# Performance work log

Measured on AMD Instinct MI355X. Metric: run time of the kernel, lower is better.

Reference implementation:

```python
import jax, jax.numpy as jnp
import numpy as np

NUM_HEADS = 8

def setup_inputs() -> dict:
    key = jax.random.key(0)
    ks = jax.random.split(key, 12)
    B, C, H, W = 4, 256, 64, 64
    QK = 256
    NSP = 256
    x = jax.random.normal(ks[0], (B, C, H, W), dtype=jnp.float32)
    affinity_matrix = jax.random.uniform(ks[1], (B, NSP, H * W), dtype=jnp.float32)
    norm_w = 1.0 + 0.02 * jax.random.normal(ks[2], (C,), dtype=jnp.float32)
    norm_b = 0.02 * jax.random.normal(ks[3], (C,), dtype=jnp.float32)
    Wq = 0.02 * jax.random.normal(ks[4], (QK, C), dtype=jnp.float32)
    Wk = 0.02 * jax.random.normal(ks[5], (QK, C), dtype=jnp.float32)
    Wv = 0.02 * jax.random.normal(ks[6], (C, C), dtype=jnp.float32)
    Wsp = 0.02 * jax.random.normal(ks[7], (QK, C), dtype=jnp.float32)
    lepe_w = 0.02 * jax.random.normal(ks[8], (C, 1, 3, 3), dtype=jnp.float32)  # depthwise OIHW
    lepe_b = 0.02 * jax.random.normal(ks[9], (C,), dtype=jnp.float32)
    return {"x": x, "affinity_matrix": affinity_matrix, "norm_w": norm_w,
            "norm_b": norm_b, "Wq": Wq, "Wk": Wk, "Wv": Wv, "Wsp": Wsp,
            "lepe_w": lepe_w, "lepe_b": lepe_b, "num_spixels": NSP}


def _layernorm2d(x, w, b, eps=1e-6):
    # LayerNorm over channel dim of NCHW input
    xp = x.transpose(0, 2, 3, 1)  # B,H,W,C
    mu = xp.mean(-1, keepdims=True)
    var = ((xp - mu) ** 2).mean(-1, keepdims=True)
    xn = (xp - mu) * jax.lax.rsqrt(var + eps) * w + b
    return xn.transpose(0, 3, 1, 2)


def _sgca(x, affinity_matrix, norm_w, norm_b, Wq, Wk, Wv, Wsp, lepe_w, lepe_b, num_spixels):
    B, C, H, W = x.shape
    HW = H * W
    h = NUM_HEADS
    qk_dim = Wq.shape[0]
    dqk = qk_dim // h
    dv = C // h
    scale = (C // h) ** -0.5

    xn = _layernorm2d(x, norm_w, norm_b)

    # superpixel aggregation: b (hw) c
    x_flat = xn.reshape(B, C, HW).transpose(0, 2, 1)  # B,HW,C
    stoken = jnp.einsum('bmn,bnc->bmc', affinity_matrix, x_flat)
    stoken = stoken / (affinity_matrix.sum(-1, keepdims=True) + 1e-16)  # B,nsp,C

    # sp projection -> B,h,dqk,nsp
    st = jnp.einsum('bmc,qc->bmq', stoken, Wsp).transpose(0, 2, 1)
    st = st.reshape(B, h, dqk, num_spixels)

    # 1x1 conv projections
    q = jnp.einsum('oc,bchw->bohw', Wq, xn).reshape(B, h, dqk, HW)
    k = jnp.einsum('oc,bchw->bohw', Wk, xn).reshape(B, h, dqk, HW)
    vx = jnp.einsum('oc,bchw->bohw', Wv, xn)  # B,C,H,W
    v = vx.reshape(B, h, dv, HW)

    # LePE: depthwise 3x3 conv on v(x)
    lepe = jax.lax.conv_general_dilated(
        vx, lepe_w, window_strides=(1, 1), padding=((1, 1), (1, 1)),
        feature_group_count=C, dimension_numbers=('NCHW', 'OIHW', 'NCHW'))
    lepe = lepe + lepe_b[None, :, None, None]
    # faithful to original: [B,C,HW] -> permute -> [B,HW,C] -> reshape B,C,H,W
    lepe = lepe.reshape(B, C, HW).transpose(0, 2, 1).reshape(B, C, H, W)

    # stage 1: k^T @ stoken, softmax over HW axis
    s_attn = jnp.einsum('bhdn,bhdm->bhnm', k, st) * scale  # B,h,HW,nsp
    s_attn = jax.nn.softmax(s_attn, axis=-2)
    s_out = jnp.einsum('bhdn,bhnm->bhdm', v, s_attn)  # B,h,dv,nsp

    # stage 2: stoken^T @ q, softmax over nsp axis
    x_attn = jnp.einsum('bhdm,bhdn->bhmn', st, q) * scale  # B,h,nsp,HW
    x_attn = jax.nn.softmax(x_attn, axis=-2)
    x_out = jnp.einsum('bhdm,bhmn->bhdn', s_out, x_attn).reshape(B, C, H, W)

    return x_out + lepe


def reference(x, affinity_matrix, norm_w, norm_b, Wq, Wk, Wv, Wsp, lepe_w, lepe_b, num_spixels):
    return _sgca(x, affinity_matrix, norm_w, norm_b, Wq, Wk, Wv, Wsp, lepe_w, lepe_b, num_spixels)
```

## Files before the change

kernel.cpp:

```cpp
#include <hip/hip_runtime.h>
#include <hip/hip_bf16.h>

#define BATCH 4
#define CCH   256
#define HWHW  4096
#define NSP   256
#define NHEAD 8
#define SCALE 0.17677669529663689f
#define PLANE 1048576L

typedef short bf16x8 __attribute__((ext_vector_type(8)));
typedef float f32x4  __attribute__((ext_vector_type(4)));

__global__ __launch_bounds__(256)
void ln_fused_kernel(const float* __restrict__ x, const float* __restrict__ w,
                     const float* __restrict__ bb,
                     const float* __restrict__ Wq, const float* __restrict__ Wk,
                     const float* __restrict__ Wv, const float* __restrict__ Wsp,
                     const float* __restrict__ aff,
                     __hip_bfloat16* __restrict__ xn_cn,
                     __hip_bfloat16* __restrict__ xn_nc,
                     __hip_bfloat16* __restrict__ wbf,
                     __hip_bfloat16* __restrict__ aff_bf)
{
    __shared__ __hip_bfloat16 xs[256][72];
    __shared__ float ps[4][64], pss[4][64], mus[64], rstds[64];
    __shared__ float wls[256], bls[256];
    int blk = blockIdx.x;
    int t = threadIdx.x;
    if (blk >= 256) {
        int sel = blk - 256;
        if (sel < 4) {
            const float* src = (sel == 0) ? Wq : (sel == 1) ? Wk : (sel == 2) ? Wv : Wsp;
            __hip_bfloat16* dst = wbf + sel * 65536;
            for (int i = t * 4; i < 65536; i += 1024) {
                float4 f = *(const float4*)(src + i);
                __hip_bfloat16 p[4];
                p[0] = __float2bfloat16(f.x); p[1] = __float2bfloat16(f.y);
                p[2] = __float2bfloat16(f.z); p[3] = __float2bfloat16(f.w);
                *(int2*)(dst + i) = *(int2*)p;
            }
        } else {
            long base = (long)(sel - 4) * 65536;
            for (int i = t * 4; i < 65536; i += 1024) {
                float4 f = *(const float4*)(aff + base + i);
                __hip_bfloat16 p[4];
                p[0] = __float2bfloat16(f.x); p[1] = __float2bfloat16(f.y);
                p[2] = __float2bfloat16(f.z); p[3] = __float2bfloat16(f.w);
                *(int2*)(aff_bf + base + i) = *(int2*)p;
            }
        }
        return;
    }
    int b = blk >> 6;
    int n0 = (blk & 63) * 64;
    int p = t & 63, cq = t >> 6;
    wls[t] = w[t]; bls[t] = bb[t];
    long base = (long)b * CCH * HWHW + n0 + p;
    float s = 0.f, ss = 0.f;
#pragma unroll 8
    for (int i = 0; i < 64; ++i) {
        int c = cq * 64 + i;
        float v = x[base + (long)c * HWHW];
        xs[c][p] = __float2bfloat16(v);
        s += v; ss += v * v;
    }
    ps[cq][p] = s; pss[cq][p] = ss;
    __syncthreads();
    if (cq == 0) {
        float S  = ps[0][p] + ps[1][p] + ps[2][p] + ps[3][p];
        float SS = pss[0][p] + pss[1][p] + pss[2][p] + pss[3][p];
        float mu = S * (1.f / 256.f);
        float var = SS * (1.f / 256.f) - mu * mu;
        mus[p] = mu; rstds[p] = rsqrtf(var + 1e-6f);
    }
    __syncthreads();
    float mu = mus[p], rstd = rstds[p];
#pragma unroll
    for (int c8 = 0; c8 < 8; ++c8) {
        short pack[8];
#pragma unroll
        for (int j = 0; j < 8; ++j) {
            int c = cq * 64 + c8 * 8 + j;
            float v = ((float)xs[c][p] - mu) * rstd * wls[c] + bls[c];
            __hip_bfloat16 bv = __float2bfloat16(v);
            xs[c][p] = bv;
            pack[j] = *(short*)&bv;
        }
        *(int4*)(xn_nc + ((long)b * HWHW + n0 + p) * CCH + cq * 64 + c8 * 8) = *(int4*)pack;
    }
    __syncthreads();
#pragma unroll
    for (int i = 0; i < 8; ++i) {
        int idx = t + i * 256;
        int c = idx >> 3, seg = idx & 7;
        *(int4*)(xn_cn + (long)(b * CCH + c) * HWHW + n0 + seg * 8) =
            *(const int4*)&xs[c][seg * 8];
    }
}

__global__ __launch_bounds__(256)
void reduce8_cast_kernel(const float* __restrict__ part, const float* __restrict__ rsPart,
                         __hip_bfloat16* __restrict__ out, float* __restrict__ rs)
{
    int i = blockIdx.x * 256 + threadIdx.x;
    if (blockIdx.x < 4) {
        int b = i >> 8, m = i & 255;
        float s = 0.f;
#pragma unroll
        for (int ch = 0; ch < 8; ++ch) s += rsPart[((b * 8 + ch) << 8) + m];
        rs[i] = s;
    }
    int b = i >> 16, idx = i & 65535;
    long base = (long)b * 8 * 65536 + idx;
    float s = 0.f;
#pragma unroll
    for (int ch = 0; ch < 8; ++ch) s += part[base + (long)ch * 65536];
    out[i] = __float2bfloat16(s);
}

template <int OUTK, bool ROWSCALE, bool ROWSUM>
__global__ __launch_bounds__(256)
void mfma_gemm_nt(const __hip_bfloat16* __restrict__ A, const __hip_bfloat16* __restrict__ B,
                  void* __restrict__ Cptr, int N, int K, int kChunk, int kShift,
                  long aStrideZ, long bStrideZ, long cStrideZ,
                  const float* __restrict__ rowScale, long sStrideZ,
                  float* __restrict__ rsPart)
{
    __shared__ __hip_bfloat16 Asm[4 * 64 * 8];
    __shared__ __hip_bfloat16 Bsm[4 * 64 * 8];
    int z = blockIdx.z;
    int b = z >> kShift;
    int ch = z & ((1 << kShift) - 1);
    int t = threadIdx.x;
    int lane = t & 63, w = t >> 6;
    int l15 = lane & 15, quad = lane >> 4;
    int Mt = blockIdx.y * 64, Nt = blockIdx.x * 64;

    const __hip_bfloat16* aSrc = A + b * aStrideZ + (long)ch * kChunk
        + (long)(Mt + w * 16 + l15) * K + quad * 8;
    const __hip_bfloat16* bSrc = B + b * bStrideZ + (long)ch * kChunk
        + (long)(Nt + w * 16 + l15) * K + quad * 8;
    __hip_bfloat16* aDst = &Asm[t * 8];
    __hip_bfloat16* bDst = &Bsm[t * 8];

    f32x4 acc00 = {0.f,0.f,0.f,0.f}, acc01 = acc00, acc10 = acc00, acc11 = acc00;
    f32x4 rs0 = acc00, rs1 = acc00;
    bf16x8 onesf;
    { short o = (l15 == 0) ? (short)0x3F80 : (short)0;
      onesf = bf16x8{o, o, o, o, o, o, o, o}; }
    int wm = (w & 1) * 2, wn = (w >> 1) * 2;

    int4 aReg = *(const int4*)aSrc;
    int4 bReg = *(const int4*)bSrc;
    for (int k0 = 0; k0 < kChunk; k0 += 32) {
        *(int4*)aDst = aReg;
        *(int4*)bDst = bReg;
        __syncthreads();
        if (k0 + 32 < kChunk) {
            aSrc += 32; bSrc += 32;
            aReg = *(const int4*)aSrc;
            bReg = *(const int4*)bSrc;
        }
        bf16x8 a0 = ((const bf16x8*)Asm)[wm * 64 + lane];
        bf16x8 a1 = ((const bf16x8*)Asm)[(wm + 1) * 64 + lane];
        bf16x8 b0 = ((const bf16x8*)Bsm)[wn * 64 + lane];
        bf16x8 b1 = ((const bf16x8*)Bsm)[(wn + 1) * 64 + lane];
        acc00 = __builtin_amdgcn_mfma_f32_16x16x32_bf16(a0, b0, acc00, 0, 0, 0);
        acc01 = __builtin_amdgcn_mfma_f32_16x16x32_bf16(a0, b1, acc01, 0, 0, 0);
        acc10 = __builtin_amdgcn_mfma_f32_16x16x32_bf16(a1, b0, acc10, 0, 0, 0);
        acc11 = __builtin_amdgcn_mfma_f32_16x16x32_bf16(a1, b1, acc11, 0, 0, 0);
        if (ROWSUM) {
            rs0 = __builtin_amdgcn_mfma_f32_16x16x32_bf16(a0, onesf, rs0, 0, 0, 0);
            rs1 = __builtin_amdgcn_mfma_f32_16x16x32_bf16(a1, onesf, rs1, 0, 0, 0);
        }
        __syncthreads();
    }
    if (ROWSUM && blockIdx.x == 0 && (w >> 1) == 0 && l15 == 0) {
#pragma unroll
        for (int r = 0; r < 4; ++r) {
            rsPart[(long)z * 256 + Mt + wm * 16 + quad * 4 + r]       = rs0[r];
            rsPart[(long)z * 256 + Mt + (wm + 1) * 16 + quad * 4 + r] = rs1[r];
        }
    }
    f32x4 accs[2][2] = {{acc00, acc01}, {acc10, acc11}};
#pragma unroll
    for (int i = 0; i < 2; ++i)
#pragma unroll
        for (int j = 0; j < 2; ++j)
#pragma unroll
            for (int r = 0; r < 4; ++r) {
                int m = Mt + (wm + i) * 16 + quad * 4 + r;
                int n = Nt + (wn + j) * 16 + l15;
                float val = accs[i][j][r];
                if (ROWSCALE) val /= (rowScale[(long)b * sStrideZ + m] + 1e-16f);
                long off = (long)z * cStrideZ + (long)m * N + n;
                if (OUTK == 0) ((float*)Cptr)[off] = val;
                else ((__hip_bfloat16*)Cptr)[off] = __float2bfloat16(val);
            }
}

__global__ __launch_bounds__(256)
void stage1_mfma(const __hip_bfloat16* __restrict__ qk_nc,
                 const __hip_bfloat16* __restrict__ v_cn,
                 const __hip_bfloat16* __restrict__ st_md,
                 __hip_bfloat16* __restrict__ opart)
{
    __shared__ __hip_bfloat16 Es[256 * 72];
    __shared__ __hip_bfloat16 sts[256 * 40];
    const int chunk = blockIdx.x, bh = blockIdx.y;
    const int b = bh >> 3, h = bh & 7;
    const int t = threadIdx.x, lane = t & 63, w = t >> 6;
    const int l15 = lane & 15, quad = lane >> 4;
    const int n0 = chunk * 256;

    {
        const int4* src = (const int4*)(st_md + ((long)(b * 256 + t)) * 256 + h * 32);
        int4* dst = (int4*)&sts[t * 40];
        dst[0] = src[0]; dst[1] = src[1]; dst[2] = src[2]; dst[3] = src[3];
    }
    __syncthreads();
    bf16x8 afrag[16];
#pragma unroll
    for (int mt = 0; mt < 16; ++mt)
        afrag[mt] = *(const bf16x8*)&sts[(mt * 16 + l15) * 40 + quad * 8];
    bf16x8 onesf;
    { short o = (l15 == 0) ? (short)0x3F80 : (short)0;
      onesf = bf16x8{o, o, o, o, o, o, o, o}; }

    f32x4 occ[4][3];
#pragma unroll
    for (int i = 0; i < 4; ++i)
#pragma unroll
        for (int j = 0; j < 3; ++j) occ[i][j] = f32x4{0.f,0.f,0.f,0.f};

    for (int sub = 0; sub < 4; ++sub) {
        const int nbase = n0 + sub * 64;
        bf16x8 kf = *(const bf16x8*)(qk_nc + ((long)b * 4096 + nbase + 16 * w + l15) * 512 + 256 + h * 32 + quad * 8);
#pragma unroll
        for (int mt = 0; mt < 16; ++mt) {
            f32x4 s = __builtin_amdgcn_mfma_f32_16x16x32_bf16(afrag[mt], kf, f32x4{0.f,0.f,0.f,0.f}, 0, 0, 0);
#pragma unroll
            for (int r = 0; r < 4; ++r)
                Es[(mt * 16 + quad * 4 + r) * 72 + 16 * w + l15] =
                    __float2bfloat16(__expf(s[r] * SCALE));
        }
        __syncthreads();
#pragma unroll
        for (int ks = 0; ks < 2; ++ks) {
            bf16x8 bf0 = *(const bf16x8*)(v_cn + ((long)(b * 256 + h * 32 + l15)) * 4096 + nbase + ks * 32 + quad * 8);
            bf16x8 bf1 = *(const bf16x8*)(v_cn + ((long)(b * 256 + h * 32 + 16 + l15)) * 4096 + nbase + ks * 32 + quad * 8);
#pragma unroll
            for (int mi = 0; mi < 4; ++mi) {
                bf16x8 af = *(const bf16x8*)&Es[(64 * w + mi * 16 + l15) * 72 + ks * 32 + quad * 8];
                occ[mi][0] = __builtin_amdgcn_mfma_f32_16x16x32_bf16(af, bf0, occ[mi][0], 0, 0, 0);
                occ[mi][1] = __builtin_amdgcn_mfma_f32_16x16x32_bf16(af, bf1, occ[mi][1], 0, 0, 0);
                occ[mi][2] = __builtin_amdgcn_mfma_f32_16x16x32_bf16(af, onesf, occ[mi][2], 0, 0, 0);
            }
        }
        __syncthreads();
    }
    __hip_bfloat16* tb = Es;
#pragma unroll
    for (int mi = 0; mi < 4; ++mi)
#pragma unroll
        for (int jt = 0; jt < 3; ++jt) {
            if (jt == 2 && l15 != 0) continue;
            int col = jt * 16 + l15;
#pragma unroll
            for (int r = 0; r < 4; ++r) {
                int m = 64 * w + mi * 16 + quad * 4 + r;
                tb[col * 264 + m] = __float2bfloat16(occ[mi][jt][r]);
            }
        }
    __syncthreads();
    int* og = (int*)(opart) + (long)(chunk * 32 + bh) * 4224;
    const int* tbi = (const int*)tb;
#pragma unroll
    for (int i = 0; i < 17; ++i) {
        int idx = t + i * 256;
        if (idx < 4224) {
            int row = idx >> 7, off = idx & 127;
            og[idx] = tbi[row * 132 + off];
        }
    }
}

__global__ __launch_bounds__(256)
void merge1_kernel(const __hip_bfloat16* __restrict__ opart, __hip_bfloat16* __restrict__ sout)
{
    int t = blockIdx.x * 256 + threadIdx.x;
    int m = t & 255;
    int d = (t >> 8) & 31;
    int bh = t >> 13;
    float num = 0.f, den = 0.f;
    for (int ch = 0; ch < 16; ++ch) {
        long base = (long)((ch * 32 + bh) * 33) * 256 + m;
        num += (float)opart[base + (long)d * 256];
        den += (float)opart[base + 32 * 256];
    }
    sout[(long)bh * 8192 + d * 256 + m] = __float2bfloat16(num / den);
}

__global__ __launch_bounds__(256)
void lepe_conv_t_kernel(const __hip_bfloat16* __restrict__ v_cn,
                        const float* __restrict__ lw, const float* __restrict__ lb,
                        __hip_bfloat16* __restrict__ lepe_cn)
{
    __shared__ __hip_bfloat16 in_t[32 * 384];
    __shared__ __hip_bfloat16 tile_bf[256 * 33];
    __shared__ float wls[288], bls[32];
    const int bx = blockIdx.x;
    const int c0 = blockIdx.y * 32;
    const int b  = blockIdx.z;
    const int t = threadIdx.x;
    const int n0 = bx * 256, r0 = bx * 4;

    for (int i = t; i < 288; i += 256) wls[i] = lw[c0 * 9 + i];
    if (t < 32)  bls[t] = lb[c0 + t];
#pragma unroll
    for (int i = 0; i < 6; ++i) {
        int vi = t + i * 256;
        int ch = vi / 48;
        int off = (vi % 48) * 8;
        int g = (r0 - 1) * 64 + off;
        int4 val = {0, 0, 0, 0};
        if ((unsigned)g < 4096u)
            val = *(const int4*)(v_cn + (((long)(b * CCH + c0 + ch)) << 12) + g);
        *(int4*)&in_t[ch * 384 + off] = val;
    }
    __syncthreads();

    const int lane = t & 63, w = t >> 6;
#pragma unroll
    for (int i = 0; i < 8; ++i) {
        int ch = w * 8 + i;
        float cr[6], lf[6], rf[6];
#pragma unroll
        for (int rr = 0; rr < 6; ++rr) {
            cr[rr] = (float)in_t[ch * 384 + rr * 64 + lane];
            float lv = __shfl_up(cr[rr], 1);
            float rv = __shfl_down(cr[rr], 1);
            lf[rr] = (lane == 0) ? 0.f : lv;
            rf[rr] = (lane == 63) ? 0.f : rv;
        }
        float w0 = wls[ch*9+0], w1 = wls[ch*9+1], w2 = wls[ch*9+2];
        float w3 = wls[ch*9+3], w4 = wls[ch*9+4], w5 = wls[ch*9+5];
        float w6 = wls[ch*9+6], w7 = wls[ch*9+7], w8 = wls[ch*9+8];
        float bias = bls[ch];
#pragma unroll
        for (int r = 0; r < 4; ++r) {
            float acc = bias
                + lf[r]   * w0 + cr[r]   * w1 + rf[r]   * w2
                + lf[r+1] * w3 + cr[r+1] * w4 + rf[r+1] * w5
                + lf[r+2] * w6 + cr[r+2] * w7 + rf[r+2] * w8;
            tile_bf[(r * 64 + lane) * 33 + ch] = __float2bfloat16(acc);
        }
    }
    __syncthreads();
#pragma unroll
    for (int i = 0; i < 32; ++i) {
        int idx = t + i * 256;
        int nl = idx >> 5, cj = idx & 31;
        int sp = n0 + nl;
        lepe_cn[((long)(b * CCH + (sp >> 4)) << 12) + (nl & 15) * 256 + c0 + cj] =
            tile_bf[nl * 33 + cj];
    }
}

__global__ __launch_bounds__(256)
void stage2_mfma(const __hip_bfloat16* __restrict__ qk_nc,
                 const __hip_bfloat16* __restrict__ st_md,
                 const __hip_bfloat16* __restrict__ sout_bf,
                 const __hip_bfloat16* __restrict__ lepe_cn,
                 float* __restrict__ out)
{
    __shared__ __hip_bfloat16 Es2[64 * 264];
    __shared__ __hip_bfloat16 sts[256 * 40];
    __shared__ __hip_bfloat16 sos[32 * 264];
    __shared__ float o_t[32 * 68];
    const int chunk = blockIdx.x, bh = blockIdx.y;
    const int b = bh >> 3, h = bh & 7;
    const int t = threadIdx.x, lane = t & 63, w = t >> 6;
    const int l15 = lane & 15, quad = lane >> 4;
    const int n0 = chunk * 256;

    {
        const int4* src = (const int4*)(st_md + ((long)(b * 256 + t)) * 256 + h * 32);
        int4* dst = (int4*)&sts[t * 40];
        dst[0] = src[0]; dst[1] = src[1]; dst[2] = src[2]; dst[3] = src[3];
    }
    {
        int row = t >> 3, seg = t & 7;
        const int4* src = (const int4*)(sout_bf + (long)bh * 8192 + row * 256 + seg * 32);
        int4* dst = (int4*)&sos[row * 264 + seg * 32];
        dst[0] = src[0]; dst[1] = src[1]; dst[2] = src[2]; dst[3] = src[3];
    }
    __syncthreads();
    bf16x8 stfrag[4];
#pragma unroll
    for (int mt = 0; mt < 4; ++mt)
        stfrag[mt] = *(const bf16x8*)&sts[(64 * w + mt * 16 + l15) * 40 + quad * 8];
    bf16x8 onesf;
    { short o = (l15 == 0) ? (short)0x3F80 : (short)0;
      onesf = bf16x8{o, o, o, o, o, o, o, o}; }

    for (int sub = 0; sub < 4; ++sub) {
        const int nbase = n0 + sub * 64;
#pragma unroll
        for (int nt = 0; nt < 4; ++nt) {
            bf16x8 qf = *(const bf16x8*)(qk_nc + ((long)b * 4096 + nbase + nt * 16 + l15) * 512 + h * 32 + quad * 8);
#pragma unroll
            for (int mt = 0; mt < 4; ++mt) {
                f32x4 s = __builtin_amdgcn_mfma_f32_16x16x32_bf16(qf, stfrag[mt], f32x4{0.f,0.f,0.f,0.f}, 0, 0, 0);
#pragma unroll
                for (int r = 0; r < 4; ++r)
                    Es2[(nt * 16 + quad * 4 + r) * 264 + 64 * w + mt * 16 + l15] =
                        __float2bfloat16(__expf(s[r] * SCALE));
            }
        }
        __syncthreads();
        f32x4 o0 = {0.f,0.f,0.f,0.f}, o1 = o0, o2 = o0;
#pragma unroll
        for (int ks = 0; ks < 8; ++ks) {
            bf16x8 af = *(const bf16x8*)&Es2[(16 * w + l15) * 264 + ks * 32 + quad * 8];
            bf16x8 b0 = *(const bf16x8*)&sos[(l15) * 264 + ks * 32 + quad * 8];
            bf16x8 b1 = *(const bf16x8*)&sos[(16 + l15) * 264 + ks * 32 + quad * 8];
            o0 = __builtin_amdgcn_mfma_f32_16x16x32_bf16(af, b0, o0, 0, 0, 0);
            o1 = __builtin_amdgcn_mfma_f32_16x16x32_bf16(af, b1, o1, 0, 0, 0);
            o2 = __builtin_amdgcn_mfma_f32_16x16x32_bf16(af, onesf, o2, 0, 0, 0);
        }
        __syncthreads();
#pragma unroll
        for (int r = 0; r < 4; ++r) {
            float den = __shfl(o2[r], lane & 48);
            float inv = 1.f / den;
            o_t[(l15) * 68 + 16 * w + quad * 4 + r]      = o0[r] * inv;
            o_t[(16 + l15) * 68 + 16 * w + quad * 4 + r] = o1[r] * inv;
        }
        __syncthreads();
        {
            int row = t >> 3, coff = (t & 7) * 8;
            long gb = ((long)(b * 256 + h * 32 + row)) * 4096 + nbase + coff;
            int4 lp4 = *(const int4*)(lepe_cn + gb);
            const __hip_bfloat16* lp = (const __hip_bfloat16*)&lp4;
            const float* sp = &o_t[row * 68 + coff];
            float4 r0, r1;
            r0.x = sp[0] + (float)lp[0]; r0.y = sp[1] + (float)lp[1];
            r0.z = sp[2] + (float)lp[2]; r0.w = sp[3] + (float)lp[3];
            r1.x = sp[4] + (float)lp[4]; r1.y = sp[5] + (float)lp[5];
            r1.z = sp[6] + (float)lp[6]; r1.w = sp[7] + (float)lp[7];
            *(float4*)(out + gb)     = r0;
            *(float4*)(out + gb + 4) = r1;
        }
        __syncthreads();
    }
}

extern "C" void kernel_launch(void* const* d_in, const int* in_sizes, int n_in,
                              void* d_out, int out_size, void* d_ws, size_t ws_size,
                              hipStream_t stream)
{
    const float* x    = (const float*)d_in[0];
    const float* aff  = (const float*)d_in[1];
    const float* nw   = (const float*)d_in[2];
    const float* nb   = (const float*)d_in[3];
    const float* Wq   = (const float*)d_in[4];
    const float* Wk   = (const float*)d_in[5];
    const float* Wv   = (const float*)d_in[6];
    const float* Wsp  = (const float*)d_in[7];
    const float* lw   = (const float*)d_in[8];
    const float* lb   = (const float*)d_in[9];
    float* out = (float*)d_out;

    float* ws = (float*)d_ws;
    const long P = PLANE;
    __hip_bfloat16* qk_nc  = (__hip_bfloat16*)(ws);
    __hip_bfloat16* v_cn   = (__hip_bfloat16*)(ws + 4 * P);
    __hip_bfloat16* xn_cn  = (__hip_bfloat16*)(ws + 6 * P);
    __hip_bfloat16* xn_nc  = (__hip_bfloat16*)(ws + 8 * P);
    __hip_bfloat16* lepe_cn= (__hip_bfloat16*)(ws + 10 * P);
    __hip_bfloat16* aff_bf = (__hip_bfloat16*)(ws + 12 * P);
    float* stoken_part = ws + 14 * P;
    __hip_bfloat16* opart = (__hip_bfloat16*)(ws + 16 * P);
    float* tail        = ws + 16 * P + 2162688;
    __hip_bfloat16* wbf       = (__hip_bfloat16*)tail;
    __hip_bfloat16* stoken_bf = (__hip_bfloat16*)(tail + 131072);
    __hip_bfloat16* st_md     = (__hip_bfloat16*)(tail + 262144);
    __hip_bfloat16* sout_bf   = (__hip_bfloat16*)(tail + 393216);
    float* rs      = tail + 524288;
    float* rs_part = tail + 525312;

    ln_fused_kernel<<<324, 256, 0, stream>>>(x, nw, nb, Wq, Wk, Wv, Wsp, aff,
                                             xn_cn, xn_nc, wbf, aff_bf);
    mfma_gemm_nt<0, false, true><<<dim3(4, 4, 32), 256, 0, stream>>>(
        aff_bf, xn_cn, stoken_part, 256, 4096, 512, 3, P, P, 65536L, nullptr, 0, rs_part);
    reduce8_cast_kernel<<<1024, 256, 0, stream>>>(stoken_part, rs_part, stoken_bf, rs);
    mfma_gemm_nt<1, true, false><<<dim3(4, 4, 4), 256, 0, stream>>>(
        stoken_bf, wbf + 3 * 65536, st_md, 256, 256, 256, 0, 65536L, 0L, 65536L, rs, 256L, nullptr);
    mfma_gemm_nt<1, false, false><<<dim3(8, 64, 4), 256, 0, stream>>>(
        xn_nc, wbf, qk_nc, 512, 256, 256, 0, P, 0L, 2 * P, nullptr, 0, nullptr);
    mfma_gemm_nt<1, false, false><<<dim3(64, 4, 4), 256, 0, stream>>>(
        wbf + 2 * 65536, xn_nc, v_cn, 4096, 256, 256, 0, 0L, P, P, nullptr, 0, nullptr);
    lepe_conv_t_kernel<<<dim3(16, 8, BATCH), 256, 0, stream>>>(v_cn, lw, lb, lepe_cn);
    stage1_mfma<<<dim3(16, 32), 256, 0, stream>>>(qk_nc, v_cn, st_md, opart);
    merge1_kernel<<<1024, 256, 0, stream>>>(opart, sout_bf);
    stage2_mfma<<<dim3(16, 32), 256, 0, stream>>>(qk_nc, st_md, sout_bf, lepe_cn, out);
}
```

Measured before the change: 212.2 us.

## Fuse affinity bf16 cast into stoken GEMM and vectorize layernorm loads

The separate fp32-to-bf16 conversion of the affinity matrix, which the layernorm kernel used to do in extra blocks, is removed. The stoken GEMM now reads fp32 affinity directly and converts it while staging into shared memory, which avoids writing and re-reading a bf16 copy. The layernorm kernel is also reorganized to use float4 loads over four pixels per thread and a shared-memory transpose for the xn_nc output. The tradeoff is that the GEMM A loads become twice as wide and the layernorm has more LDS traffic for the transposed write.

Result: slower. 217.6 us (+2.5%).

```diff
diff --git a/kernel.cpp b/kernel.cpp
--- a/kernel.cpp
+++ b/kernel.cpp
@@ -17,77 +17,72 @@
                      const float* __restrict__ bb,
                      const float* __restrict__ Wq, const float* __restrict__ Wk,
                      const float* __restrict__ Wv, const float* __restrict__ Wsp,
-                     const float* __restrict__ aff,
                      __hip_bfloat16* __restrict__ xn_cn,
                      __hip_bfloat16* __restrict__ xn_nc,
-                     __hip_bfloat16* __restrict__ wbf,
-                     __hip_bfloat16* __restrict__ aff_bf)
-{
-    __shared__ __hip_bfloat16 xs[256][72];
-    __shared__ float ps[4][64], pss[4][64], mus[64], rstds[64];
+                     __hip_bfloat16* __restrict__ wbf)
+{
+    __shared__ __hip_bfloat16 xs[256][80];
+    __shared__ float ps[16][64], pss[16][64];
+    __shared__ float mus[64], rstds[64];
     __shared__ float wls[256], bls[256];
     int blk = blockIdx.x;
     int t = threadIdx.x;
     if (blk >= 256) {
         int sel = blk - 256;
-        if (sel < 4) {
-            const float* src = (sel == 0) ? Wq : (sel == 1) ? Wk : (sel == 2) ? Wv : Wsp;
-            __hip_bfloat16* dst = wbf + sel * 65536;
-            for (int i = t * 4; i < 65536; i += 1024) {
-                float4 f = *(const float4*)(src + i);
-                __hip_bfloat16 p[4];
-                p[0] = __float2bfloat16(f.x); p[1] = __float2bfloat16(f.y);
-                p[2] = __float2bfloat16(f.z); p[3] = __float2bfloat16(f.w);
-                *(int2*)(dst + i) = *(int2*)p;
-            }
-        } else {
-            long base = (long)(sel - 4) * 65536;
-            for (int i = t * 4; i < 65536; i += 1024) {
-                float4 f = *(const float4*)(aff + base + i);
-                __hip_bfloat16 p[4];
-                p[0] = __float2bfloat16(f.x); p[1] = __float2bfloat16(f.y);
-                p[2] = __float2bfloat16(f.z); p[3] = __float2bfloat16(f.w);
-                *(int2*)(aff_bf + base + i) = *(int2*)p;
-            }
+        const float* src = (sel == 0) ? Wq : (sel == 1) ? Wk : (sel == 2) ? Wv : Wsp;
+        __hip_bfloat16* dst = wbf + sel * 65536;
+        for (int i = t * 4; i < 65536; i += 1024) {
+            float4 f = *(const float4*)(src + i);
+            __hip_bfloat16 p[4];
+            p[0] = __float2bfloat16(f.x); p[1] = __float2bfloat16(f.y);
+            p[2] = __float2bfloat16(f.z); p[3] = __float2bfloat16(f.w);
+            *(int2*)(dst + i) = *(int2*)p;
         }
         return;
     }
     int b = blk >> 6;
     int n0 = (blk & 63) * 64;
-    int p = t & 63, cq = t >> 6;
+    int px4 = t & 15, cg = t >> 4;
     wls[t] = w[t]; bls[t] = bb[t];
-    long base = (long)b * CCH * HWHW + n0 + p;
-    float s = 0.f, ss = 0.f;
-#pragma unroll 8
-    for (int i = 0; i < 64; ++i) {
-        int c = cq * 64 + i;
-        float v = x[base + (long)c * HWHW];
-        xs[c][p] = __float2bfloat16(v);
-        s += v; ss += v * v;
-    }
-    ps[cq][p] = s; pss[cq][p] = ss;
-    __syncthreads();
-    if (cq == 0) {
-        float S  = ps[0][p] + ps[1][p] + ps[2][p] + ps[3][p];
-        float SS = pss[0][p] + pss[1][p] + pss[2][p] + pss[3][p];
+    long base = (long)b * CCH * HWHW + n0 + px4 * 4;
+    float s0 = 0.f, s1 = 0.f, s2 = 0.f, s3 = 0.f;
+    float q0 = 0.f, q1 = 0.f, q2 = 0.f, q3 = 0.f;
+#pragma unroll
+    for (int j = 0; j < 16; ++j) {
+        int c = cg * 16 + j;
+        float4 f = *(const float4*)(x + base + (long)c * HWHW);
+        s0 += f.x; s1 += f.y; s2 += f.z; s3 += f.w;
+        q0 += f.x * f.x; q1 += f.y * f.y; q2 += f.z * f.z; q3 += f.w * f.w;
+        __hip_bfloat16 p[4];
+        p[0] = __float2bfloat16(f.x); p[1] = __float2bfloat16(f.y);
+        p[2] = __float2bfloat16(f.z); p[3] = __float2bfloat16(f.w);
+        *(int2*)&xs[c][px4 * 4] = *(int2*)p;
+    }
+    *(float4*)&ps[cg][px4 * 4]  = float4{s0, s1, s2, s3};
+    *(float4*)&pss[cg][px4 * 4] = float4{q0, q1, q2, q3};
+    __syncthreads();
+    if (t < 64) {
+        float S = 0.f, SS = 0.f;
+#pragma unroll
+        for (int g = 0; g < 16; ++g) { S += ps[g][t]; SS += pss[g][t]; }
         float mu = S * (1.f / 256.f);
         float var = SS * (1.f / 256.f) - mu * mu;
-        mus[p] = mu; rstds[p] = rsqrtf(var + 1e-6f);
-    }
-    __syncthreads();
-    float mu = mus[p], rstd = rstds[p];
-#pragma unroll
-    for (int c8 = 0; c8 < 8; ++c8) {
-        short pack[8];
-#pragma unroll
-        for (int j = 0; j < 8; ++j) {
-            int c = cq * 64 + c8 * 8 + j;
-            float v = ((float)xs[c][p] - mu) * rstd * wls[c] + bls[c];
-            __hip_bfloat16 bv = __float2bfloat16(v);
-            xs[c][p] = bv;
-            pack[j] = *(short*)&bv;
-        }
-        *(int4*)(xn_nc + ((long)b * HWHW + n0 + p) * CCH + cq * 64 + c8 * 8) = *(int4*)pack;
+        mus[t] = mu; rstds[t] = rsqrtf(var + 1e-6f);
+    }
+    __syncthreads();
+    float mu[4], rst[4];
+#pragma unroll
+    for (int i = 0; i < 4; ++i) { mu[i] = mus[px4 * 4 + i]; rst[i] = rstds[px4 * 4 + i]; }
+#pragma unroll
+    for (int j = 0; j < 16; ++j) {
+        int c = cg * 16 + j;
+        __hip_bfloat16 p[4];
+        *(int2*)p = *(const int2*)&xs[c][px4 * 4];
+        float wc = wls[c], bc = bls[c];
+#pragma unroll
+        for (int i = 0; i < 4; ++i)
+            p[i] = __float2bfloat16(((float)p[i] - mu[i]) * rst[i] * wc + bc);
+        *(int2*)&xs[c][px4 * 4] = *(int2*)p;
     }
     __syncthreads();
 #pragma unroll
@@ -97,6 +92,18 @@
         *(int4*)(xn_cn + (long)(b * CCH + c) * HWHW + n0 + seg * 8) =
             *(const int4*)&xs[c][seg * 8];
     }
+#pragma unroll
+    for (int i = 0; i < 8; ++i) {
+        int idx = t + i * 256;
+        int px = idx >> 5, g8 = idx & 31;
+        short pack[8];
+#pragma unroll
+        for (int j = 0; j < 8; ++j) {
+            __hip_bfloat16 v = xs[g8 * 8 + j][px];
+            pack[j] = *(short*)&v;
+        }
+        *(int4*)(xn_nc + ((long)b * HWHW + n0 + px) * CCH + g8 * 8) = *(int4*)pack;
+    }
 }
 
 __global__ __launch_bounds__(256)
@@ -119,9 +126,9 @@
     out[i] = __float2bfloat16(s);
 }
 
-template <int OUTK, bool ROWSCALE, bool ROWSUM>
-__global__ __launch_bounds__(256)
-void mfma_gemm_nt(const __hip_bfloat16* __restrict__ A, const __hip_bfloat16* __restrict__ B,
+template <int OUTK, bool ROWSCALE, bool A32, bool ROWSUM>
+__global__ __launch_bounds__(256)
+void mfma_gemm_nt(const void* __restrict__ Aptr, const __hip_bfloat16* __restrict__ B,
                   void* __restrict__ Cptr, int N, int K, int kChunk, int kShift,
                   long aStrideZ, long bStrideZ, long cStrideZ,
                   const float* __restrict__ rowScale, long sStrideZ,
@@ -137,8 +144,11 @@
     int l15 = lane & 15, quad = lane >> 4;
     int Mt = blockIdx.y * 64, Nt = blockIdx.x * 64;
 
-    const __hip_bfloat16* aSrc = A + b * aStrideZ + (long)ch * kChunk
-        + (long)(Mt + w * 16 + l15) * K + quad * 8;
+    const float* aSrcF = A32 ? ((const float*)Aptr + b * aStrideZ + (long)ch * kChunk
+                                + (long)(Mt + w * 16 + l15) * K + quad * 8) : nullptr;
+    const __hip_bfloat16* aSrcB = A32 ? nullptr :
+        ((const __hip_bfloat16*)Aptr + b * aStrideZ + (long)ch * kChunk
+         + (long)(Mt + w * 16 + l15) * K + quad * 8);
     const __hip_bfloat16* bSrc = B + b * bStrideZ + (long)ch * kChunk
         + (long)(Nt + w * 16 + l15) * K + quad * 8;
     __hip_bfloat16* aDst = &Asm[t * 8];
@@ -151,15 +161,28 @@
       onesf = bf16x8{o, o, o, o, o, o, o, o}; }
     int wm = (w & 1) * 2, wn = (w >> 1) * 2;
 
-    int4 aReg = *(const int4*)aSrc;
-    int4 bReg = *(const int4*)bSrc;
+    float4 aF0, aF1; int4 aReg, bReg;
+    if (A32) { aF0 = ((const float4*)aSrcF)[0]; aF1 = ((const float4*)aSrcF)[1]; }
+    else aReg = *(const int4*)aSrcB;
+    bReg = *(const int4*)bSrc;
+
     for (int k0 = 0; k0 < kChunk; k0 += 32) {
-        *(int4*)aDst = aReg;
+        if (A32) {
+            __hip_bfloat16 tmp[8];
+            tmp[0]=__float2bfloat16(aF0.x); tmp[1]=__float2bfloat16(aF0.y);
+            tmp[2]=__float2bfloat16(aF0.z); tmp[3]=__float2bfloat16(aF0.w);
+            tmp[4]=__float2bfloat16(aF1.x); tmp[5]=__float2bfloat16(aF1.y);
+            tmp[6]=__float2bfloat16(aF1.z); tmp[7]=__float2bfloat16(aF1.w);
+            *(int4*)aDst = *(const int4*)tmp;
+        } else {
+            *(int4*)aDst = aReg;
+        }
         *(int4*)bDst = bReg;
         __syncthreads();
         if (k0 + 32 < kChunk) {
-            aSrc += 32; bSrc += 32;
-            aReg = *(const int4*)aSrc;
+            bSrc += 32;
+            if (A32) { aSrcF += 32; aF0 = ((const float4*)aSrcF)[0]; aF1 = ((const float4*)aSrcF)[1]; }
+            else     { aSrcB += 32; aReg = *(const int4*)aSrcB; }
             bReg = *(const int4*)bSrc;
         }
         bf16x8 a0 = ((const bf16x8*)Asm)[wm * 64 + lane];
@@ -480,10 +503,9 @@
     __hip_bfloat16* xn_cn  = (__hip_bfloat16*)(ws + 6 * P);
     __hip_bfloat16* xn_nc  = (__hip_bfloat16*)(ws + 8 * P);
     __hip_bfloat16* lepe_cn= (__hip_bfloat16*)(ws + 10 * P);
-    __hip_bfloat16* aff_bf = (__hip_bfloat16*)(ws + 12 * P);
-    float* stoken_part = ws + 14 * P;
-    __hip_bfloat16* opart = (__hip_bfloat16*)(ws + 16 * P);
-    float* tail        = ws + 16 * P + 2162688;
+    float* stoken_part = ws + 12 * P;
+    __hip_bfloat16* opart = (__hip_bfloat16*)(ws + 14 * P);
+    float* tail        = ws + 14 * P + 2162688;
     __hip_bfloat16* wbf       = (__hip_bfloat16*)tail;
     __hip_bfloat16* stoken_bf = (__hip_bfloat16*)(tail + 131072);
     __hip_bfloat16* st_md     = (__hip_bfloat16*)(tail + 262144);
@@ -491,16 +513,16 @@
     float* rs      = tail + 524288;
     float* rs_part = tail + 525312;
 
-    ln_fused_kernel<<<324, 256, 0, stream>>>(x, nw, nb, Wq, Wk, Wv, Wsp, aff,
-                                             xn_cn, xn_nc, wbf, aff_bf);
-    mfma_gemm_nt<0, false, true><<<dim3(4, 4, 32), 256, 0, stream>>>(
-        aff_bf, xn_cn, stoken_part, 256, 4096, 512, 3, P, P, 65536L, nullptr, 0, rs_part);
+    ln_fused_kernel<<<260, 256, 0, stream>>>(x, nw, nb, Wq, Wk, Wv, Wsp,
+                                             xn_cn, xn_nc, wbf);
+    mfma_gemm_nt<0, false, true, true><<<dim3(4, 4, 32), 256, 0, stream>>>(
+        aff, xn_cn, stoken_part, 256, 4096, 512, 3, P, P, 65536L, nullptr, 0, rs_part);
     reduce8_cast_kernel<<<1024, 256, 0, stream>>>(stoken_part, rs_part, stoken_bf, rs);
-    mfma_gemm_nt<1, true, false><<<dim3(4, 4, 4), 256, 0, stream>>>(
+    mfma_gemm_nt<1, true, false, false><<<dim3(4, 4, 4), 256, 0, stream>>>(
         stoken_bf, wbf + 3 * 65536, st_md, 256, 256, 256, 0, 65536L, 0L, 65536L, rs, 256L, nullptr);
-    mfma_gemm_nt<1, false, false><<<dim3(8, 64, 4), 256, 0, stream>>>(
+    mfma_gemm_nt<1, false, false, false><<<dim3(8, 64, 4), 256, 0, stream>>>(
         xn_nc, wbf, qk_nc, 512, 256, 256, 0, P, 0L, 2 * P, nullptr, 0, nullptr);
-    mfma_gemm_nt<1, false, false><<<dim3(64, 4, 4), 256, 0, stream>>>(
+    mfma_gemm_nt<1, false, false, false><<<dim3(64, 4, 4), 256, 0, stream>>>(
         wbf + 2 * 65536, xn_nc, v_cn, 4096, 256, 256, 0, 0L, P, P, nullptr, 0, nullptr);
     lepe_conv_t_kernel<<<dim3(16, 8, BATCH), 256, 0, stream>>>(v_cn, lw, lb, lepe_cn);
     stage1_mfma<<<dim3(16, 32), 256, 0, stream>>>(qk_nc, v_cn, st_md, opart);
```
